# Kernel optimization log

Measured on AMD Instinct MI355X. Metric: run time of the kernel, lower is better.

The kernel has to match this reference:

```python
import jax, jax.numpy as jnp
import numpy as np

N, S, R, CM = 1, 128, 256, 256
C, CZ = 32, 128


def setup_inputs() -> dict:
    key = jax.random.key(0)
    k1, k2, k3, k4 = jax.random.split(key, 4)
    return {
        "msa_repr": jax.random.normal(k1, (N, S, R, CM), dtype=jnp.float32),
        "left_proj": jax.random.normal(k2, (CM, C), dtype=jnp.float32) * 0.05,
        "right_proj": jax.random.normal(k3, (CM, C), dtype=jnp.float32) * 0.05,
        "out_proj": jax.random.normal(k4, (C * C, CZ), dtype=jnp.float32) * 0.05,
    }


def reference(msa_repr, left_proj, right_proj, out_proj):
    # msa_repr: [N, S, R, CM]
    # Project to left/right activations and move R before S
    # (equivalent to torch matmul + transpose(-2, -3)).
    a = jnp.einsum("nsrm,mc->nrsc", msa_repr, left_proj)   # [N, R, S, C]
    b = jnp.einsum("nsrm,mc->nrsc", msa_repr, right_proj)  # [N, R, S, C]
    # Outer product contracted over the MSA dim S:
    # outer[n, r, t, c, e] = sum_s a[n, r, s, c] * b[n, t, s, e]
    outer = jnp.einsum("nrsc,ntse->nrtce", a, b)            # [N, R, R, C, C]
    n, r, t = outer.shape[:3]
    outer = outer.reshape(n, r, t, C * C)                   # [N, R, R, C*C]
    # Output projection to pair channels cz
    return outer @ out_proj                                 # [N, R, R, CZ]
```

## Files before the change

kernel.cpp:

```cpp
#include <hip/hip_runtime.h>

typedef __bf16 bf16x8 __attribute__((ext_vector_type(8)));
typedef __bf16 bf16x4 __attribute__((ext_vector_type(4)));
typedef float f32x16 __attribute__((ext_vector_type(16)));
typedef float f32x4 __attribute__((ext_vector_type(4)));

constexpr int S = 128, R = 256, CM = 256, C = 32, CZ = 128;

#define MFMA __builtin_amdgcn_mfma_f32_32x32x16_bf16

__device__ __forceinline__ bf16x4 cvt4(float a, float b, float c, float d) {
    bf16x4 r;
    r[0] = (__bf16)a; r[1] = (__bf16)b; r[2] = (__bf16)c; r[3] = (__bf16)d;
    return r;
}

__global__ __launch_bounds__(256) void k_wt(const float* __restrict__ W,
                                            __bf16* __restrict__ WTf) {
    int g = blockIdx.x * 256 + threadIdx.x;
    int cz = g & 127;
    int k = g >> 7;
    int e = k >> 5, c = k & 31;
    float v = W[(size_t)(c * 32 + e) * 128 + cz];
    WTf[((size_t)(k >> 3) * 128 + cz) * 8 + (k & 7)] = (__bf16)v;
}

__global__ __launch_bounds__(256) void k_wlr(const float* __restrict__ Lp,
                                             const float* __restrict__ Rp,
                                             __bf16* __restrict__ WLRT) {
    int c = blockIdx.x;
    int m = threadIdx.x;
    const float* src = (c < 32) ? Lp : Rp;
    WLRT[(size_t)c * 256 + m] = (__bf16)src[(size_t)m * 32 + (c & 31)];
}

__global__ __launch_bounds__(256) void k_proj(const float* __restrict__ msa,
                                              const __bf16* __restrict__ WLRT,
                                              __bf16* __restrict__ aTf,
                                              __bf16* __restrict__ bTf) {
    __shared__ __align__(16) __bf16 As[64 * 256];
    const int r = blockIdx.x;
    const int sh = blockIdx.y;
    const int t = threadIdx.x;

#pragma unroll 4
    for (int it = 0; it < 16; ++it) {
        int idx = it * 256 + t;
        int row = idx >> 6;
        int cg = idx & 63;
        float4 v = *(const float4*)&msa[((size_t)(sh * 64 + row) * R + r) * CM + cg * 4];
        bf16x4 h = cvt4(v.x, v.y, v.z, v.w);
        int P = (cg >> 1) ^ (row & 15);
        *(bf16x4*)((char*)As + row * 512 + P * 16 + (cg & 1) * 8) = h;
    }
    __syncthreads();

    const int w = t >> 6;
    const int l31 = t & 31;
    const int kh = (t >> 5) & 1;
    const int sd = w & 1;
    const int mi = w >> 1;

    f32x16 acc;
#pragma unroll
    for (int q = 0; q < 16; ++q) acc[q] = 0.f;

    const bf16x8* wb = (const bf16x8*)&WLRT[(size_t)(sd * 32 + l31) * 256 + 8 * kh];
    const int srow = mi * 32 + l31;
    const char* arow = (const char*)As + srow * 512;

    __builtin_amdgcn_s_setprio(1);
#pragma unroll
    for (int ks = 0; ks < 16; ++ks) {
        int P = (2 * ks + kh) ^ (srow & 15);
        bf16x8 af = *(const bf16x8*)(arow + P * 16);
        acc = MFMA(af, wb[2 * ks], acc, 0, 0, 0);
    }
    __builtin_amdgcn_s_setprio(0);

    __bf16* dst = sd ? bTf : aTf;
    const int wg = sh * 2 + mi;
#pragma unroll
    for (int q = 0; q < 4; ++q) {
        size_t base = (size_t)r * 4096 + (size_t)(2 * wg + (q >> 1)) * 512 +
                      (size_t)(q & 1) * 256 + (size_t)l31 * 8 + 4 * kh;
        *(bf16x4*)&dst[base] = cvt4(acc[4 * q + 0], acc[4 * q + 1],
                                    acc[4 * q + 2], acc[4 * q + 3]);
    }
}

__global__ __launch_bounds__(512, 2) void k_main(const __bf16* __restrict__ aTf,
                                                 const __bf16* __restrict__ bTf,
                                                 const __bf16* __restrict__ WTf,
                                                 float* __restrict__ out) {
    __shared__ __align__(16) __bf16 Gs[64 * 1024];

    const int t = threadIdx.x;
    const int w = t >> 6;
    const int l = t & 63;
    const int lane = l & 31;
    const int kh = l >> 5;
    const int r0 = blockIdx.x * 8;
    const int t0 = blockIdx.y * 8;

    const int rg = w >> 1;
    const int tg = w & 1;

    f32x16 acc[2][4];
#pragma unroll
    for (int i = 0; i < 2; ++i)
#pragma unroll
        for (int j = 0; j < 4; ++j)
#pragma unroll
            for (int q = 0; q < 16; ++q) acc[i][j][q] = 0.f;

    const bf16x8* ap0 = (const bf16x8*)aTf + ((size_t)(r0 + 2 * rg + 0) * 512 + kh * 32 + lane);
    const bf16x8* ap1 = (const bf16x8*)aTf + ((size_t)(r0 + 2 * rg + 1) * 512 + kh * 32 + lane);
    const bf16x8* bp0 = (const bf16x8*)bTf + ((size_t)(t0 + 4 * tg + 0) * 512 + kh * 32 + lane);
    const bf16x8* bp1 = (const bf16x8*)bTf + ((size_t)(t0 + 4 * tg + 1) * 512 + kh * 32 + lane);
    const bf16x8* bp2 = (const bf16x8*)bTf + ((size_t)(t0 + 4 * tg + 2) * 512 + kh * 32 + lane);
    const bf16x8* bp3 = (const bf16x8*)bTf + ((size_t)(t0 + 4 * tg + 3) * 512 + kh * 32 + lane);

    bf16x8 A0[2], B0[4], A1[2], B1[4];
#define LDA(Aa, Bb, ks) do { \
    Aa[0] = ap0[(ks) * 64]; Aa[1] = ap1[(ks) * 64]; \
    Bb[0] = bp0[(ks) * 64]; Bb[1] = bp1[(ks) * 64]; \
    Bb[2] = bp2[(ks) * 64]; Bb[3] = bp3[(ks) * 64]; } while (0)
#define PH_A(Aa, Bb) do { \
    __builtin_amdgcn_s_setprio(1); \
    acc[0][0] = MFMA(Aa[0], Bb[0], acc[0][0], 0, 0, 0); \
    acc[0][1] = MFMA(Aa[0], Bb[1], acc[0][1], 0, 0, 0); \
    acc[0][2] = MFMA(Aa[0], Bb[2], acc[0][2], 0, 0, 0); \
    acc[0][3] = MFMA(Aa[0], Bb[3], acc[0][3], 0, 0, 0); \
    acc[1][0] = MFMA(Aa[1], Bb[0], acc[1][0], 0, 0, 0); \
    acc[1][1] = MFMA(Aa[1], Bb[1], acc[1][1], 0, 0, 0); \
    acc[1][2] = MFMA(Aa[1], Bb[2], acc[1][2], 0, 0, 0); \
    acc[1][3] = MFMA(Aa[1], Bb[3], acc[1][3], 0, 0, 0); \
    __builtin_amdgcn_s_setprio(0); } while (0)

    LDA(A0, B0, 0);
#pragma unroll
    for (int ks = 0; ks < 8; ks += 2) {
        LDA(A1, B1, ks + 1);
        PH_A(A0, B0);
        LDA(A0, B0, (ks + 2) & 7);
        PH_A(A1, B1);
    }

#pragma unroll
    for (int i = 0; i < 2; ++i) {
#pragma unroll
        for (int j = 0; j < 4; ++j) {
            int p = (2 * rg + i) * 8 + 4 * tg + j;
            unsigned prow = (unsigned)p * 2048;
#pragma unroll
            for (int q = 0; q < 4; ++q) {
                int Lc = lane * 4 + q;
                int P = Lc ^ (p & 15) ^ (lane & 7);
                *(bf16x4*)((char*)Gs + prow + (unsigned)P * 16 + kh * 8) =
                    cvt4(acc[i][j][4 * q + 0], acc[i][j][4 * q + 1],
                         acc[i][j][4 * q + 2], acc[i][j][4 * q + 3]);
            }
        }
    }
    __syncthreads();

    const int kq = w >> 1;
    const int ng = w & 1;
    const int czl0 = ng * 64 + lane;
    const int czl1 = czl0 + 32;
    const bf16x8* wb0 = (const bf16x8*)WTf + ((size_t)kh * 128 + czl0);
    const bf16x8* wb1 = (const bf16x8*)WTf + ((size_t)kh * 128 + czl1);
    const unsigned prow0 = (unsigned)lane * 2048;
    const unsigned prow1 = (unsigned)(lane + 32) * 2048;
    const int p15 = lane & 15;

    f32x16 o00, o01, o10, o11;
#pragma unroll
    for (int q = 0; q < 16; ++q) { o00[q] = 0.f; o01[q] = 0.f; o10[q] = 0.f; o11[q] = 0.f; }

    bf16x8 Wa0, Wa1, Ga0, Ga1, Wb0_, Wb1_, Gb0, Gb1;
#define LDB(W0v, W1v, G0v, G1v, kk) do { \
    W0v = wb0[(size_t)(kk) * 256]; \
    W1v = wb1[(size_t)(kk) * 256]; \
    int Lr = (kk) * 2 + kh; \
    int P = Lr ^ p15 ^ ((Lr >> 2) & 7); \
    G0v = *(const bf16x8*)((const char*)Gs + prow0 + (unsigned)P * 16); \
    G1v = *(const bf16x8*)((const char*)Gs + prow1 + (unsigned)P * 16); } while (0)
#define PHB(W0v, W1v, G0v, G1v) do { \
    __builtin_amdgcn_s_setprio(1); \
    o00 = MFMA(G0v, W0v, o00, 0, 0, 0); \
    o01 = MFMA(G0v, W1v, o01, 0, 0, 0); \
    o10 = MFMA(G1v, W0v, o10, 0, 0, 0); \
    o11 = MFMA(G1v, W1v, o11, 0, 0, 0); \
    __builtin_amdgcn_s_setprio(0); } while (0)

    LDB(Wa0, Wa1, Ga0, Ga1, kq * 16);
#pragma unroll
    for (int j = 0; j < 16; j += 2) {
        LDB(Wb0_, Wb1_, Gb0, Gb1, kq * 16 + ((j + 1) & 15));
        PHB(Wa0, Wa1, Ga0, Ga1);
        LDB(Wa0, Wa1, Ga0, Ga1, kq * 16 + ((j + 2) & 15));
        PHB(Wb0_, Wb1_, Gb0, Gb1);
    }
    __syncthreads();

    {
        char* pr = (char*)Gs + (size_t)w * 16384;
        const f32x16* os[4] = {&o00, &o01, &o10, &o11};
#pragma unroll
        for (int s2 = 0; s2 < 4; ++s2) {
#pragma unroll
            for (int pc = 0; pc < 4; ++pc) {
                f32x4 v;
                v[0] = (*os[s2])[4 * pc + 0]; v[1] = (*os[s2])[4 * pc + 1];
                v[2] = (*os[s2])[4 * pc + 2]; v[3] = (*os[s2])[4 * pc + 3];
                *(f32x4*)(pr + ((s2 * 4 + pc) * 64 + l) * 16) = v;
            }
        }
    }
    __syncthreads();

    {
        const int ngx = w >> 2;
        const int mix = (w >> 1) & 1;
        const int nix = w & 1;
        const int s2 = mix * 2 + nix;
        f32x16 sm;
#pragma unroll
        for (int q = 0; q < 16; ++q) sm[q] = 0.f;
#pragma unroll
        for (int kq2 = 0; kq2 < 4; ++kq2) {
            const char* pr = (const char*)Gs + (size_t)(kq2 * 2 + ngx) * 16384;
#pragma unroll
            for (int pc = 0; pc < 4; ++pc) {
                f32x4 v = *(const f32x4*)(pr + ((s2 * 4 + pc) * 64 + l) * 16);
                sm[4 * pc + 0] += v[0]; sm[4 * pc + 1] += v[1];
                sm[4 * pc + 2] += v[2]; sm[4 * pc + 3] += v[3];
            }
        }
        const int czl = ngx * 64 + nix * 32 + (l & 31);
        const int khx = l >> 5;
#pragma unroll
        for (int reg = 0; reg < 16; ++reg) {
            int pl = mix * 32 + (reg & 3) + 8 * (reg >> 2) + 4 * khx;
            int prr = pl >> 3, ptt = pl & 7;
            out[((size_t)(r0 + prr) * 256 + (t0 + ptt)) * 128 + czl] = sm[reg];
        }
    }
}

extern "C" void kernel_launch(void* const* d_in, const int* in_sizes, int n_in,
                              void* d_out, int out_size, void* d_ws, size_t ws_size,
                              hipStream_t stream) {
    const float* msa = (const float*)d_in[0];
    const float* left = (const float*)d_in[1];
    const float* right = (const float*)d_in[2];
    const float* W = (const float*)d_in[3];

    __bf16* aTf = (__bf16*)d_ws;
    __bf16* bTf = aTf + (size_t)R * 4096;
    __bf16* WTf = bTf + (size_t)R * 4096;
    __bf16* WLRT = WTf + (size_t)128 * 1024;
    float* outp = (float*)d_out;

    k_wt<<<512, 256, 0, stream>>>(W, WTf);
    k_wlr<<<64, 256, 0, stream>>>(left, right, WLRT);
    k_proj<<<dim3(256, 2), 256, 0, stream>>>(msa, WLRT, aTf, bTf);
    k_main<<<dim3(32, 32), 512, 0, stream>>>(aTf, bTf, WTf, outp);
}
```

Measured before the change: 60.61 us.

## Double threads per block in projection and main kernels with split-K reductions

The projection kernel moves to 512 threads and splits the K loop across two wave halves, combining partial sums through shared memory. The main kernel moves to 1024 threads with 16 waves, so each wave computes fewer outer-product tiles and fewer output-projection accumulators. The final reduction now runs only on the kq==0 waves and adds three partials. The aim is more waves in flight and lower register pressure per wave to hide latency. In exchange it adds shared-memory round trips and barriers, and a 1024-thread block of k_main still needs 128 KB of shared memory.

```diff
diff --git a/kernel.cpp b/kernel.cpp
--- a/kernel.cpp
+++ b/kernel.cpp
@@ -34,18 +34,19 @@
     WLRT[(size_t)c * 256 + m] = (__bf16)src[(size_t)m * 32 + (c & 31)];
 }
 
-__global__ __launch_bounds__(256) void k_proj(const float* __restrict__ msa,
+__global__ __launch_bounds__(512) void k_proj(const float* __restrict__ msa,
                                               const __bf16* __restrict__ WLRT,
                                               __bf16* __restrict__ aTf,
                                               __bf16* __restrict__ bTf) {
     __shared__ __align__(16) __bf16 As[64 * 256];
+    __shared__ __align__(16) char Pp[4 * 4096];
     const int r = blockIdx.x;
     const int sh = blockIdx.y;
     const int t = threadIdx.x;
 
-#pragma unroll 4
-    for (int it = 0; it < 16; ++it) {
-        int idx = it * 256 + t;
+#pragma unroll
+    for (int it = 0; it < 8; ++it) {
+        int idx = it * 512 + t;
         int row = idx >> 6;
         int cg = idx & 63;
         float4 v = *(const float4*)&msa[((size_t)(sh * 64 + row) * R + r) * CM + cg * 4];
@@ -56,10 +57,12 @@
     __syncthreads();
 
     const int w = t >> 6;
+    const int l = t & 63;
     const int l31 = t & 31;
     const int kh = (t >> 5) & 1;
-    const int sd = w & 1;
-    const int mi = w >> 1;
+    const int ksh = w >> 2;
+    const int sd = (w >> 1) & 1;
+    const int mi = w & 1;
 
     f32x16 acc;
 #pragma unroll
@@ -71,28 +74,48 @@
 
     __builtin_amdgcn_s_setprio(1);
 #pragma unroll
-    for (int ks = 0; ks < 16; ++ks) {
+    for (int j = 0; j < 8; ++j) {
+        int ks = ksh * 8 + j;
         int P = (2 * ks + kh) ^ (srow & 15);
         bf16x8 af = *(const bf16x8*)(arow + P * 16);
         acc = MFMA(af, wb[2 * ks], acc, 0, 0, 0);
     }
     __builtin_amdgcn_s_setprio(0);
 
-    __bf16* dst = sd ? bTf : aTf;
-    const int wg = sh * 2 + mi;
-#pragma unroll
-    for (int q = 0; q < 4; ++q) {
-        size_t base = (size_t)r * 4096 + (size_t)(2 * wg + (q >> 1)) * 512 +
-                      (size_t)(q & 1) * 256 + (size_t)l31 * 8 + 4 * kh;
-        *(bf16x4*)&dst[base] = cvt4(acc[4 * q + 0], acc[4 * q + 1],
-                                    acc[4 * q + 2], acc[4 * q + 3]);
-    }
-}
-
-__global__ __launch_bounds__(512, 2) void k_main(const __bf16* __restrict__ aTf,
-                                                 const __bf16* __restrict__ bTf,
-                                                 const __bf16* __restrict__ WTf,
-                                                 float* __restrict__ out) {
+    char* pbase = Pp + (size_t)(sd * 2 + mi) * 4096;
+    if (ksh == 1) {
+#pragma unroll
+        for (int pc = 0; pc < 4; ++pc) {
+            f32x4 v;
+            v[0] = acc[4 * pc + 0]; v[1] = acc[4 * pc + 1];
+            v[2] = acc[4 * pc + 2]; v[3] = acc[4 * pc + 3];
+            *(f32x4*)(pbase + ((pc * 64) + l) * 16) = v;
+        }
+    }
+    __syncthreads();
+    if (ksh == 0) {
+#pragma unroll
+        for (int pc = 0; pc < 4; ++pc) {
+            f32x4 v = *(const f32x4*)(pbase + ((pc * 64) + l) * 16);
+            acc[4 * pc + 0] += v[0]; acc[4 * pc + 1] += v[1];
+            acc[4 * pc + 2] += v[2]; acc[4 * pc + 3] += v[3];
+        }
+        __bf16* dst = sd ? bTf : aTf;
+        const int wg = sh * 2 + mi;
+#pragma unroll
+        for (int q = 0; q < 4; ++q) {
+            size_t base = (size_t)r * 4096 + (size_t)(2 * wg + (q >> 1)) * 512 +
+                          (size_t)(q & 1) * 256 + (size_t)l31 * 8 + 4 * kh;
+            *(bf16x4*)&dst[base] = cvt4(acc[4 * q + 0], acc[4 * q + 1],
+                                        acc[4 * q + 2], acc[4 * q + 3]);
+        }
+    }
+}
+
+__global__ __launch_bounds__(1024, 4) void k_main(const __bf16* __restrict__ aTf,
+                                                  const __bf16* __restrict__ bTf,
+                                                  const __bf16* __restrict__ WTf,
+                                                  float* __restrict__ out) {
     __shared__ __align__(16) __bf16 Gs[64 * 1024];
 
     const int t = threadIdx.x;
@@ -103,39 +126,32 @@
     const int r0 = blockIdx.x * 8;
     const int t0 = blockIdx.y * 8;
 
-    const int rg = w >> 1;
-    const int tg = w & 1;
-
-    f32x16 acc[2][4];
+    const int rg = w >> 2;
+    const int tg = w & 3;
+
+    f32x16 acc[2][2];
 #pragma unroll
     for (int i = 0; i < 2; ++i)
 #pragma unroll
-        for (int j = 0; j < 4; ++j)
+        for (int j = 0; j < 2; ++j)
 #pragma unroll
             for (int q = 0; q < 16; ++q) acc[i][j][q] = 0.f;
 
     const bf16x8* ap0 = (const bf16x8*)aTf + ((size_t)(r0 + 2 * rg + 0) * 512 + kh * 32 + lane);
     const bf16x8* ap1 = (const bf16x8*)aTf + ((size_t)(r0 + 2 * rg + 1) * 512 + kh * 32 + lane);
-    const bf16x8* bp0 = (const bf16x8*)bTf + ((size_t)(t0 + 4 * tg + 0) * 512 + kh * 32 + lane);
-    const bf16x8* bp1 = (const bf16x8*)bTf + ((size_t)(t0 + 4 * tg + 1) * 512 + kh * 32 + lane);
-    const bf16x8* bp2 = (const bf16x8*)bTf + ((size_t)(t0 + 4 * tg + 2) * 512 + kh * 32 + lane);
-    const bf16x8* bp3 = (const bf16x8*)bTf + ((size_t)(t0 + 4 * tg + 3) * 512 + kh * 32 + lane);
-
-    bf16x8 A0[2], B0[4], A1[2], B1[4];
+    const bf16x8* bp0 = (const bf16x8*)bTf + ((size_t)(t0 + 2 * tg + 0) * 512 + kh * 32 + lane);
+    const bf16x8* bp1 = (const bf16x8*)bTf + ((size_t)(t0 + 2 * tg + 1) * 512 + kh * 32 + lane);
+
+    bf16x8 A0[2], B0[2], A1[2], B1[2];
 #define LDA(Aa, Bb, ks) do { \
     Aa[0] = ap0[(ks) * 64]; Aa[1] = ap1[(ks) * 64]; \
-    Bb[0] = bp0[(ks) * 64]; Bb[1] = bp1[(ks) * 64]; \
-    Bb[2] = bp2[(ks) * 64]; Bb[3] = bp3[(ks) * 64]; } while (0)
+    Bb[0] = bp0[(ks) * 64]; Bb[1] = bp1[(ks) * 64]; } while (0)
 #define PH_A(Aa, Bb) do { \
     __builtin_amdgcn_s_setprio(1); \
     acc[0][0] = MFMA(Aa[0], Bb[0], acc[0][0], 0, 0, 0); \
     acc[0][1] = MFMA(Aa[0], Bb[1], acc[0][1], 0, 0, 0); \
-    acc[0][2] = MFMA(Aa[0], Bb[2], acc[0][2], 0, 0, 0); \
-    acc[0][3] = MFMA(Aa[0], Bb[3], acc[0][3], 0, 0, 0); \
     acc[1][0] = MFMA(Aa[1], Bb[0], acc[1][0], 0, 0, 0); \
     acc[1][1] = MFMA(Aa[1], Bb[1], acc[1][1], 0, 0, 0); \
-    acc[1][2] = MFMA(Aa[1], Bb[2], acc[1][2], 0, 0, 0); \
-    acc[1][3] = MFMA(Aa[1], Bb[3], acc[1][3], 0, 0, 0); \
     __builtin_amdgcn_s_setprio(0); } while (0)
 
     LDA(A0, B0, 0);
@@ -150,8 +166,8 @@
 #pragma unroll
     for (int i = 0; i < 2; ++i) {
 #pragma unroll
-        for (int j = 0; j < 4; ++j) {
-            int p = (2 * rg + i) * 8 + 4 * tg + j;
+        for (int j = 0; j < 2; ++j) {
+            int p = (2 * rg + i) * 8 + 2 * tg + j;
             unsigned prow = (unsigned)p * 2048;
 #pragma unroll
             for (int q = 0; q < 4; ++q) {
@@ -165,87 +181,79 @@
     }
     __syncthreads();
 
-    const int kq = w >> 1;
+    const int kq = w >> 2;
+    const int mt = (w >> 1) & 1;
     const int ng = w & 1;
     const int czl0 = ng * 64 + lane;
     const int czl1 = czl0 + 32;
     const bf16x8* wb0 = (const bf16x8*)WTf + ((size_t)kh * 128 + czl0);
     const bf16x8* wb1 = (const bf16x8*)WTf + ((size_t)kh * 128 + czl1);
-    const unsigned prow0 = (unsigned)lane * 2048;
-    const unsigned prow1 = (unsigned)(lane + 32) * 2048;
+    const unsigned prowG = (unsigned)(mt * 32 + lane) * 2048;
     const int p15 = lane & 15;
 
-    f32x16 o00, o01, o10, o11;
-#pragma unroll
-    for (int q = 0; q < 16; ++q) { o00[q] = 0.f; o01[q] = 0.f; o10[q] = 0.f; o11[q] = 0.f; }
-
-    bf16x8 Wa0, Wa1, Ga0, Ga1, Wb0_, Wb1_, Gb0, Gb1;
-#define LDB(W0v, W1v, G0v, G1v, kk) do { \
+    f32x16 o0, o1;
+#pragma unroll
+    for (int q = 0; q < 16; ++q) { o0[q] = 0.f; o1[q] = 0.f; }
+
+    bf16x8 Wa0, Wa1, Ga, Wb0_, Wb1_, Gb;
+#define LDB(W0v, W1v, Gv, kk) do { \
     W0v = wb0[(size_t)(kk) * 256]; \
     W1v = wb1[(size_t)(kk) * 256]; \
     int Lr = (kk) * 2 + kh; \
     int P = Lr ^ p15 ^ ((Lr >> 2) & 7); \
-    G0v = *(const bf16x8*)((const char*)Gs + prow0 + (unsigned)P * 16); \
-    G1v = *(const bf16x8*)((const char*)Gs + prow1 + (unsigned)P * 16); } while (0)
-#define PHB(W0v, W1v, G0v, G1v) do { \
+    Gv = *(const bf16x8*)((const char*)Gs + prowG + (unsigned)P * 16); } while (0)
+#define PHB(W0v, W1v, Gv) do { \
     __builtin_amdgcn_s_setprio(1); \
-    o00 = MFMA(G0v, W0v, o00, 0, 0, 0); \
-    o01 = MFMA(G0v, W1v, o01, 0, 0, 0); \
-    o10 = MFMA(G1v, W0v, o10, 0, 0, 0); \
-    o11 = MFMA(G1v, W1v, o11, 0, 0, 0); \
+    o0 = MFMA(Gv, W0v, o0, 0, 0, 0); \
+    o1 = MFMA(Gv, W1v, o1, 0, 0, 0); \
     __builtin_amdgcn_s_setprio(0); } while (0)
 
-    LDB(Wa0, Wa1, Ga0, Ga1, kq * 16);
+    LDB(Wa0, Wa1, Ga, kq * 16);
 #pragma unroll
     for (int j = 0; j < 16; j += 2) {
-        LDB(Wb0_, Wb1_, Gb0, Gb1, kq * 16 + ((j + 1) & 15));
-        PHB(Wa0, Wa1, Ga0, Ga1);
-        LDB(Wa0, Wa1, Ga0, Ga1, kq * 16 + ((j + 2) & 15));
-        PHB(Wb0_, Wb1_, Gb0, Gb1);
-    }
-    __syncthreads();
-
-    {
-        char* pr = (char*)Gs + (size_t)w * 16384;
-        const f32x16* os[4] = {&o00, &o01, &o10, &o11};
-#pragma unroll
-        for (int s2 = 0; s2 < 4; ++s2) {
+        LDB(Wb0_, Wb1_, Gb, kq * 16 + ((j + 1) & 15));
+        PHB(Wa0, Wa1, Ga);
+        LDB(Wa0, Wa1, Ga, kq * 16 + ((j + 2) & 15));
+        PHB(Wb0_, Wb1_, Gb);
+    }
+    __syncthreads();
+
+    if (kq > 0) {
+        char* pr = (char*)Gs + (size_t)((kq - 1) * 4 + mt * 2 + ng) * 8192;
+#pragma unroll
+        for (int oi = 0; oi < 2; ++oi) {
+            const f32x16& ov = oi ? o1 : o0;
 #pragma unroll
             for (int pc = 0; pc < 4; ++pc) {
                 f32x4 v;
-                v[0] = (*os[s2])[4 * pc + 0]; v[1] = (*os[s2])[4 * pc + 1];
-                v[2] = (*os[s2])[4 * pc + 2]; v[3] = (*os[s2])[4 * pc + 3];
-                *(f32x4*)(pr + ((s2 * 4 + pc) * 64 + l) * 16) = v;
+                v[0] = ov[4 * pc + 0]; v[1] = ov[4 * pc + 1];
+                v[2] = ov[4 * pc + 2]; v[3] = ov[4 * pc + 3];
+                *(f32x4*)(pr + ((oi * 4 + pc) * 64 + l) * 16) = v;
             }
         }
     }
     __syncthreads();
 
-    {
-        const int ngx = w >> 2;
-        const int mix = (w >> 1) & 1;
-        const int nix = w & 1;
-        const int s2 = mix * 2 + nix;
-        f32x16 sm;
-#pragma unroll
-        for (int q = 0; q < 16; ++q) sm[q] = 0.f;
-#pragma unroll
-        for (int kq2 = 0; kq2 < 4; ++kq2) {
-            const char* pr = (const char*)Gs + (size_t)(kq2 * 2 + ngx) * 16384;
+    if (kq == 0) {
+#pragma unroll
+        for (int kq2 = 1; kq2 < 4; ++kq2) {
+            const char* pr = (const char*)Gs + (size_t)((kq2 - 1) * 4 + mt * 2 + ng) * 8192;
 #pragma unroll
             for (int pc = 0; pc < 4; ++pc) {
-                f32x4 v = *(const f32x4*)(pr + ((s2 * 4 + pc) * 64 + l) * 16);
-                sm[4 * pc + 0] += v[0]; sm[4 * pc + 1] += v[1];
-                sm[4 * pc + 2] += v[2]; sm[4 * pc + 3] += v[3];
+                f32x4 v0 = *(const f32x4*)(pr + ((pc) * 64 + l) * 16);
+                f32x4 v1 = *(const f32x4*)(pr + ((4 + pc) * 64 + l) * 16);
+                o0[4 * pc + 0] += v0[0]; o0[4 * pc + 1] += v0[1];
+                o0[4 * pc + 2] += v0[2]; o0[4 * pc + 3] += v0[3];
+                o1[4 * pc + 0] += v1[0]; o1[4 * pc + 1] += v1[1];
+                o1[4 * pc + 2] += v1[2]; o1[4 * pc + 3] += v1[3];
             }
         }
-        const int czl = ngx * 64 + nix * 32 + (l & 31);
-        const int khx = l >> 5;
 #pragma unroll
         for (int reg = 0; reg < 16; ++reg) {
-            int pl = mix * 32 + (reg & 3) + 8 * (reg >> 2) + 4 * khx;
-            int prr = pl >> 3, ptt = pl & 7;
-            out[((size_t)(r0 + prr) * 256 + (t0 + ptt)) * 128 + czl] = sm[reg];
+            int pl = mt * 32 + (reg & 3) + 8 * (reg >> 2) + 4 * kh;
+            int pr2 = pl >> 3, pt = pl & 7;
+            out[((size_t)(r0 + pr2) * 256 + (t0 + pt)) * 128 + czl0] = o0[reg];
+            out[((size_t)(r0 + pr2) * 256 + (t0 + pt)) * 128 + czl1] = o1[reg];
         }
     }
 }
@@ -266,6 +274,6 @@
 
     k_wt<<<512, 256, 0, stream>>>(W, WTf);
     k_wlr<<<64, 256, 0, stream>>>(left, right, WLRT);
-    k_proj<<<dim3(256, 2), 256, 0, stream>>>(msa, WLRT, aTf, bTf);
-    k_main<<<dim3(32, 32), 512, 0, stream>>>(aTf, bTf, WTf, outp);
-}
+    k_proj<<<dim3(256, 2), 512, 0, stream>>>(msa, WLRT, aTf, bTf);
+    k_main<<<dim3(32, 32), 1024, 0, stream>>>(aTf, bTf, WTf, outp);
+}
```

Result: slower. 66.95 us (+10.5%).
